# Optimization experiments

Hardware: AMD Instinct MI355X
Metric: run time of the kernel (lower is better)

Reference implementation:

```python
import jax, jax.numpy as jnp
import numpy as np

N_TOKENS = 16384
HIDDEN = 1024
FFN = 256
N_EXPERTS = 12
TOP_K = 3


def setup_inputs() -> dict:
    key = jax.random.key(0)
    ks = jax.random.split(key, 5)
    return {
        "hidden_states": jax.random.normal(ks[0], (N_TOKENS, HIDDEN), dtype=jnp.float32),
        "gate_w": jax.random.normal(ks[1], (N_EXPERTS, HIDDEN), dtype=jnp.float32) * 0.02,
        "w1": jax.random.normal(ks[2], (N_EXPERTS, FFN, HIDDEN), dtype=jnp.float32) * 0.02,
        "w2": jax.random.normal(ks[3], (N_EXPERTS, HIDDEN, FFN), dtype=jnp.float32) * 0.02,
        "w3": jax.random.normal(ks[4], (N_EXPERTS, FFN, HIDDEN), dtype=jnp.float32) * 0.02,
    }


def reference(hidden_states, gate_w, w1, w2, w3):
    # Eval mode: no jitter noise (module only applies it when self.training).
    n = hidden_states.shape[0]
    router_logits = hidden_states @ gate_w.T                       # [N, E]
    routing_weights = jax.nn.softmax(router_logits.astype(jnp.float32), axis=1)
    top_w, selected_experts = jax.lax.top_k(routing_weights, TOP_K)  # [N, K]
    top_w = top_w / jnp.sum(top_w, axis=-1, keepdims=True)
    top_w = top_w.astype(hidden_states.dtype)

    # Dense combine-weight matrix [N, E]: zero for unselected experts.
    combine = jnp.zeros((n, N_EXPERTS), dtype=hidden_states.dtype)
    combine = combine.at[jnp.arange(n)[:, None], selected_experts].add(top_w)

    # SwiGLU experts computed for all (token, expert) pairs; unselected pairs
    # are zeroed by the combine weights -> same math as gather/scatter loop.
    h1 = jnp.einsum('nd,efd->nef', hidden_states, w1)              # [N, E, F]
    h3 = jnp.einsum('nd,efd->nef', hidden_states, w3)              # [N, E, F]
    h = jax.nn.silu(h1) * h3
    h = h * combine[:, :, None]                                    # weight before combine
    final = jnp.einsum('nef,edf->nd', h, w2)                       # [N, D]

    flat_e = selected_experts.reshape(-1)
    flat_w = top_w.reshape(-1).astype(jnp.float32)
    importance = jnp.zeros((N_EXPERTS,), jnp.float32).at[flat_e].add(flat_w)
    # torch.std is unbiased (ddof=1)
    router_loss = jnp.std(importance, ddof=1)
    return final, router_logits, selected_experts, router_loss
```

## Files before the change

kernel.cpp:

```cpp
#include <hip/hip_runtime.h>
#include <hip/hip_bf16.h>

#define NT 16384
#define HID 1024
#define FFN_ 256
#define NE 12
#define TOPK 3

typedef float  float4x  __attribute__((ext_vector_type(4)));
typedef short  short8x  __attribute__((ext_vector_type(8)));

__device__ __forceinline__ unsigned short f2bf(float f) {
    unsigned u = __float_as_uint(f);
    u += 0x7fffu + ((u >> 16) & 1u);
    return (unsigned short)(u >> 16);
}
__device__ __forceinline__ float bf2f(unsigned short u) {
    return __uint_as_float(((unsigned)u) << 16);
}

__device__ __forceinline__ void gl2lds16(const void* g, void* l) {
    __builtin_amdgcn_global_load_lds(
        (const __attribute__((address_space(1))) unsigned int*)g,
        (__attribute__((address_space(3))) unsigned int*)l, 16, 0, 0);
}

__global__ __launch_bounds__(256) void router_cvt_kernel(
    const float* __restrict__ X, const float* __restrict__ G,
    const float* __restrict__ w1, const float* __restrict__ w3, const float* __restrict__ w2,
    unsigned short* __restrict__ o1, unsigned short* __restrict__ o3, unsigned short* __restrict__ o2,
    float* __restrict__ out_logits, float* __restrict__ out_sel,
    unsigned short* __restrict__ xb,
    int* __restrict__ sel_e, float* __restrict__ sel_w)
{
    __shared__ __align__(16) float gls[NE * HID];

    if (blockIdx.x < 768) {
        const float* s; unsigned short* d;
        int m = blockIdx.x >> 8;
        if (m == 0)      { s = w1; d = o1; }
        else if (m == 1) { s = w3; d = o3; }
        else             { s = w2; d = o2; }
        const int n4 = NE * FFN_ * HID / 4;
        for (int i = (blockIdx.x & 255) * 256 + threadIdx.x; i < n4; i += 65536) {
            float4 v = ((const float4*)s)[i];
            ushort4 o;
            o.x = f2bf(v.x); o.y = f2bf(v.y); o.z = f2bf(v.z); o.w = f2bf(v.w);
            ((ushort4*)d)[i] = o;
        }
        return;
    }

    const int bx = blockIdx.x - 768;
    for (int i = threadIdx.x; i < NE * HID / 4; i += 256)
        ((float4*)gls)[i] = ((const float4*)G)[i];
    __syncthreads();

    const int wave = threadIdx.x >> 6, lane = threadIdx.x & 63;
    const int t = bx * 4 + wave;

    float xr[16];
    const float* xt = X + (size_t)t * HID;
    unsigned short* xbt = xb + (size_t)t * HID;
#pragma unroll
    for (int j = 0; j < 4; j++) {
        float4 v = ((const float4*)xt)[j * 64 + lane];
        xr[j*4+0] = v.x; xr[j*4+1] = v.y; xr[j*4+2] = v.z; xr[j*4+3] = v.w;
        ushort4 o;
        o.x = f2bf(v.x); o.y = f2bf(v.y); o.z = f2bf(v.z); o.w = f2bf(v.w);
        ((ushort4*)xbt)[j * 64 + lane] = o;
    }

    float logit[NE];
#pragma unroll
    for (int e = 0; e < NE; e++) {
        float s = 0.f;
#pragma unroll
        for (int j = 0; j < 4; j++) {
            float4 g = ((const float4*)gls)[e * 256 + j * 64 + lane];
            s += xr[j*4+0]*g.x + xr[j*4+1]*g.y + xr[j*4+2]*g.z + xr[j*4+3]*g.w;
        }
#pragma unroll
        for (int d = 32; d; d >>= 1) s += __shfl_xor(s, d, 64);
        logit[e] = s;
    }

    if (lane == 0) {
        float m = logit[0];
#pragma unroll
        for (int e = 1; e < NE; e++) m = fmaxf(m, logit[e]);
#pragma unroll
        for (int e = 0; e < NE; e++) out_logits[(size_t)t * NE + e] = logit[e];

        bool used[NE];
#pragma unroll
        for (int e = 0; e < NE; e++) used[e] = false;
        int   sel[TOPK];
        float w[TOPK];
        float wsum = 0.f;
#pragma unroll
        for (int k = 0; k < TOPK; k++) {
            int best = -1; float bv = -1e30f;
            for (int e = 0; e < NE; e++)
                if (!used[e] && logit[e] > bv) { bv = logit[e]; best = e; }
            used[best] = true;
            sel[k] = best;
            w[k] = __expf(bv - m);
            wsum += w[k];
        }
        float inv = 1.f / wsum;
#pragma unroll
        for (int k = 0; k < TOPK; k++) {
            float wk = w[k] * inv;
            out_sel[(size_t)t * TOPK + k] = (float)sel[k];
            sel_e[t * TOPK + k] = sel[k];
            sel_w[t * TOPK + k] = wk;
        }
    }
}

__global__ __launch_bounds__(256) void hist_kernel(
    const int* __restrict__ sel_e, const float* __restrict__ sel_w,
    int* __restrict__ counts, float* __restrict__ importance)
{
    __shared__ int   lcnt[NE];
    __shared__ float limp[NE];
    const int tid = threadIdx.x;
    if (tid < NE) { lcnt[tid] = 0; limp[tid] = 0.f; }
    __syncthreads();
    const int t = blockIdx.x * 256 + tid;
#pragma unroll
    for (int k = 0; k < TOPK; k++) {
        int e = sel_e[t * TOPK + k];
        atomicAdd(&lcnt[e], 1);
        atomicAdd(&limp[e], sel_w[t * TOPK + k]);
    }
    __syncthreads();
    if (tid < NE) {
        atomicAdd(&counts[tid], lcnt[tid]);
        atomicAdd(&importance[tid], limp[tid]);
    }
}

__global__ void scan_loss(const int* __restrict__ counts, int* __restrict__ cursor,
                          int* __restrict__ offsets, int* __restrict__ tile_base,
                          const float* __restrict__ importance,
                          float* __restrict__ loss_out)
{
    if (threadIdx.x == 0) {
        int acc = 0, tb = 0;
        for (int e = 0; e < NE; e++) {
            offsets[e] = acc; cursor[e] = acc; tile_base[e] = tb;
            tb += (counts[e] + 127) >> 7;
            acc += counts[e];
        }
        offsets[NE] = acc;
        tile_base[NE] = tb;
        float mean = 0.f;
        for (int e = 0; e < NE; e++) mean += importance[e];
        mean /= (float)NE;
        float var = 0.f;
        for (int e = 0; e < NE; e++) { float d = importance[e] - mean; var += d * d; }
        var /= (float)(NE - 1);
        *loss_out = sqrtf(var);
    }
}

__global__ __launch_bounds__(256) void place_kernel(
    const int* __restrict__ sel_e, const float* __restrict__ sel_w,
    int* __restrict__ cursor, int* __restrict__ tok_ids, float* __restrict__ slot_w,
    int* __restrict__ inv3)
{
    __shared__ int lcnt[NE];
    __shared__ int lbase[NE];
    const int tid = threadIdx.x;
    if (tid < NE) lcnt[tid] = 0;
    __syncthreads();
    const int t = blockIdx.x * 256 + tid;
    int e[TOPK], r[TOPK];
#pragma unroll
    for (int k = 0; k < TOPK; k++) {
        e[k] = sel_e[t * TOPK + k];
        r[k] = atomicAdd(&lcnt[e[k]], 1);
    }
    __syncthreads();
    if (tid < NE) lbase[tid] = atomicAdd(&cursor[tid], lcnt[tid]);
    __syncthreads();
#pragma unroll
    for (int k = 0; k < TOPK; k++) {
        int pos = lbase[e[k]] + r[k];
        tok_ids[pos] = t;
        slot_w[pos] = sel_w[t * TOPK + k];
        inv3[t * TOPK + k] = pos;
    }
}

__global__ __launch_bounds__(256) void ffn1_kernel(
    const unsigned short* __restrict__ xb, const unsigned short* __restrict__ wb1,
    const unsigned short* __restrict__ wb3, const int* __restrict__ offsets,
    const int* __restrict__ tile_base,
    const int* __restrict__ tok_ids, const float* __restrict__ slot_w,
    unsigned short* __restrict__ H)
{
    const int bx = blockIdx.x;
    if (bx >= tile_base[NE]) return;
    int e = 0;
    while (bx >= tile_base[e + 1]) e++;
    const int base = offsets[e];
    const int count = offsets[e + 1] - base;
    const int m0 = (bx - tile_base[e]) << 7;
    const int n0 = blockIdx.y * 128;

    __shared__ __align__(16) unsigned short As[2][4096];
    __shared__ __align__(16) unsigned short B1s[2][4096];
    __shared__ __align__(16) unsigned short B3s[2][4096];
    __shared__ int   tids[128];
    __shared__ float wts[128];

    const int tid = threadIdx.x;
    if (tid < 128) {
        int s = m0 + tid;
        tids[tid] = (s < count) ? tok_ids[base + s] : 0;
        wts[tid]  = (s < count) ? slot_w[base + s] : 0.f;
    }
    __syncthreads();

    const int wave = tid >> 6, lane = tid & 63;
    const int wave_m = wave & 1, wave_n = wave >> 1;

    const int srow = wave * 32 + (lane >> 2);
    const int schunk = (((lane & 3) ^ ((srow >> 1) & 3)) << 3);
    const int tokA0 = tids[srow];
    const int tokA1 = tids[srow + 16];

    const unsigned short* asrc0 = xb + (size_t)tokA0 * HID + schunk;
    const unsigned short* asrc1 = xb + (size_t)tokA1 * HID + schunk;
    const unsigned short* b1p0 = wb1 + (size_t)(e * FFN_ + n0 + srow) * HID + schunk;
    const unsigned short* b1p1 = b1p0 + 16 * HID;
    const unsigned short* b3p0 = wb3 + (size_t)(e * FFN_ + n0 + srow) * HID + schunk;
    const unsigned short* b3p1 = b3p0 + 16 * HID;

    const int woff = wave * 2048;

#define FFN1_STAGE(p) do {                                             \
        char* aD  = (char*)&As[p][0]  + woff;                          \
        char* b1D = (char*)&B1s[p][0] + woff;                          \
        char* b3D = (char*)&B3s[p][0] + woff;                          \
        gl2lds16(asrc0, aD);  gl2lds16(asrc1, aD + 1024);              \
        gl2lds16(b1p0, b1D);  gl2lds16(b1p1, b1D + 1024);              \
        gl2lds16(b3p0, b3D);  gl2lds16(b3p1, b3D + 1024);              \
        asrc0 += 32; asrc1 += 32; b1p0 += 32; b1p1 += 32;              \
        b3p0 += 32; b3p1 += 32; } while (0)

    const int r15 = lane & 15;
    const int rchunk = (((lane >> 4) ^ ((r15 >> 1) & 3)) << 3);

    float4x acc1[4][4], acc3[4][4];
#pragma unroll
    for (int mi = 0; mi < 4; mi++)
#pragma unroll
        for (int ni = 0; ni < 4; ni++) {
            acc1[mi][ni] = (float4x){0.f, 0.f, 0.f, 0.f};
            acc3[mi][ni] = (float4x){0.f, 0.f, 0.f, 0.f};
        }

    FFN1_STAGE(0);
    for (int kk = 0; kk < HID / 32; kk++) {
        __syncthreads();
        if (kk + 1 < HID / 32) FFN1_STAGE((kk + 1) & 1);
        const int p = kk & 1;

        short8x a[4], b1f[4], b3f[4];
#pragma unroll
        for (int mi = 0; mi < 4; mi++)
            a[mi] = *(const short8x*)(&As[p][0] + (wave_m * 64 + mi * 16 + r15) * 32 + rchunk);
#pragma unroll
        for (int ni = 0; ni < 4; ni++) {
            b1f[ni] = *(const short8x*)(&B1s[p][0] + (wave_n * 64 + ni * 16 + r15) * 32 + rchunk);
            b3f[ni] = *(const short8x*)(&B3s[p][0] + (wave_n * 64 + ni * 16 + r15) * 32 + rchunk);
        }
#pragma unroll
        for (int mi = 0; mi < 4; mi++)
#pragma unroll
            for (int ni = 0; ni < 4; ni++) {
                acc1[mi][ni] = __builtin_amdgcn_mfma_f32_16x16x32_bf16(a[mi], b1f[ni], acc1[mi][ni], 0, 0, 0);
                acc3[mi][ni] = __builtin_amdgcn_mfma_f32_16x16x32_bf16(a[mi], b3f[ni], acc3[mi][ni], 0, 0, 0);
            }
    }
#undef FFN1_STAGE

    const int laneh = lane >> 4;
#pragma unroll
    for (int mi = 0; mi < 4; mi++)
#pragma unroll
        for (int ni = 0; ni < 4; ni++)
#pragma unroll
            for (int r = 0; r < 4; r++) {
                int ml = wave_m * 64 + mi * 16 + laneh * 4 + r;
                int s = m0 + ml;
                if (s < count) {
                    float v1 = acc1[mi][ni][r];
                    float v3 = acc3[mi][ni][r];
                    float h = v1 * (1.f / (1.f + __expf(-v1))) * v3 * wts[ml];
                    int n = n0 + wave_n * 64 + ni * 16 + r15;
                    H[(size_t)(base + s) * FFN_ + n] = f2bf(h);
                }
            }
}

__global__ __launch_bounds__(256) void ffn2_store(
    const unsigned short* __restrict__ H, const unsigned short* __restrict__ wb2,
    const int* __restrict__ offsets, const int* __restrict__ tile_base,
    unsigned short* __restrict__ Obuf, int co, int nc)
{
    const int bx = blockIdx.x;
    if (bx >= tile_base[NE]) return;
    int e = 0;
    while (bx >= tile_base[e + 1]) e++;
    const int base = offsets[e];
    const int count = offsets[e + 1] - base;
    const int m0 = (bx - tile_base[e]) << 7;
    const int n0g = co + blockIdx.y * 128;

    __shared__ __align__(16) unsigned short As[2][4096];
    __shared__ __align__(16) unsigned short Bs[2][4096];

    const int tid = threadIdx.x;
    const int wave = tid >> 6, lane = tid & 63;
    const int wave_m = wave & 1, wave_n = wave >> 1;

    const int srow = wave * 32 + (lane >> 2);
    const int schunk = (((lane & 3) ^ ((srow >> 1) & 3)) << 3);

    const unsigned short* a0 = H + (size_t)(base + m0 + srow) * FFN_ + schunk;
    const unsigned short* a1 = a0 + 16 * FFN_;
    const unsigned short* b0 = wb2 + (size_t)(e * HID + n0g + srow) * FFN_ + schunk;
    const unsigned short* b1 = b0 + 16 * FFN_;

    const int woff = wave * 2048;

#define FFN2_STAGE(p) do {                                             \
        char* aD = (char*)&As[p][0] + woff;                            \
        char* bD = (char*)&Bs[p][0] + woff;                            \
        gl2lds16(a0, aD);  gl2lds16(a1, aD + 1024);                    \
        gl2lds16(b0, bD);  gl2lds16(b1, bD + 1024);                    \
        a0 += 32; a1 += 32; b0 += 32; b1 += 32; } while (0)

    const int r15 = lane & 15;
    const int rchunk = (((lane >> 4) ^ ((r15 >> 1) & 3)) << 3);

    float4x acc[4][4];
#pragma unroll
    for (int mi = 0; mi < 4; mi++)
#pragma unroll
        for (int ni = 0; ni < 4; ni++) acc[mi][ni] = (float4x){0.f, 0.f, 0.f, 0.f};

    FFN2_STAGE(0);
    for (int kk = 0; kk < FFN_ / 32; kk++) {
        __syncthreads();
        if (kk + 1 < FFN_ / 32) FFN2_STAGE((kk + 1) & 1);
        const int p = kk & 1;

        short8x af[4], bf[4];
#pragma unroll
        for (int mi = 0; mi < 4; mi++)
            af[mi] = *(const short8x*)(&As[p][0] + (wave_m * 64 + mi * 16 + r15) * 32 + rchunk);
#pragma unroll
        for (int ni = 0; ni < 4; ni++)
            bf[ni] = *(const short8x*)(&Bs[p][0] + (wave_n * 64 + ni * 16 + r15) * 32 + rchunk);
#pragma unroll
        for (int mi = 0; mi < 4; mi++)
#pragma unroll
            for (int ni = 0; ni < 4; ni++)
                acc[mi][ni] = __builtin_amdgcn_mfma_f32_16x16x32_bf16(af[mi], bf[ni], acc[mi][ni], 0, 0, 0);
    }
#undef FFN2_STAGE

    const int laneh = lane >> 4;
#pragma unroll
    for (int mi = 0; mi < 4; mi++)
#pragma unroll
        for (int ni = 0; ni < 4; ni++)
#pragma unroll
            for (int r = 0; r < 4; r++) {
                int ml = wave_m * 64 + mi * 16 + laneh * 4 + r;
                int s = m0 + ml;
                if (s < count) {
                    int col = (n0g - co) + wave_n * 64 + ni * 16 + r15;
                    Obuf[(size_t)(base + s) * nc + col] = f2bf(acc[mi][ni][r]);
                }
            }
}

__global__ __launch_bounds__(256) void combine_kernel(
    const unsigned short* __restrict__ Obuf, const int* __restrict__ inv3,
    float* __restrict__ final_out, int co, int pt_shift)
{
    const int idx = blockIdx.x * 256 + threadIdx.x;
    const int per_t = 1 << pt_shift;
    const int t = idx >> pt_shift;
    const int c4 = idx & (per_t - 1);
    const int s0 = inv3[t * TOPK + 0];
    const int s1 = inv3[t * TOPK + 1];
    const int s2 = inv3[t * TOPK + 2];
    const ushort4* O = (const ushort4*)Obuf;
    ushort4 u0 = O[(size_t)s0 * per_t + c4];
    ushort4 u1 = O[(size_t)s1 * per_t + c4];
    ushort4 u2 = O[(size_t)s2 * per_t + c4];
    float4 r;
    r.x = bf2f(u0.x) + bf2f(u1.x) + bf2f(u2.x);
    r.y = bf2f(u0.y) + bf2f(u1.y) + bf2f(u2.y);
    r.z = bf2f(u0.z) + bf2f(u1.z) + bf2f(u2.z);
    r.w = bf2f(u0.w) + bf2f(u1.w) + bf2f(u2.w);
    ((float4*)(final_out + (size_t)t * HID + co))[c4] = r;
}

__global__ __launch_bounds__(256) void ffn2_atomic(
    const unsigned short* __restrict__ H, const unsigned short* __restrict__ wb2,
    const int* __restrict__ offsets, const int* __restrict__ tile_base,
    const int* __restrict__ tok_ids, float* __restrict__ final_out)
{
    const int bx = blockIdx.x;
    if (bx >= tile_base[NE]) return;
    int e = 0;
    while (bx >= tile_base[e + 1]) e++;
    const int base = offsets[e];
    const int count = offsets[e + 1] - base;
    const int m0 = (bx - tile_base[e]) << 7;
    const int n0 = blockIdx.y * 128;

    __shared__ __align__(16) unsigned short As[2][4096];
    __shared__ __align__(16) unsigned short Bs[2][4096];
    __shared__ int tids[128];

    const int tid = threadIdx.x;
    if (tid < 128) {
        int s = m0 + tid;
        tids[tid] = (s < count) ? tok_ids[base + s] : 0;
    }
    __syncthreads();

    const int wave = tid >> 6, lane = tid & 63;
    const int wave_m = wave & 1, wave_n = wave >> 1;

    const int srow = wave * 32 + (lane >> 2);
    const int schunk = (((lane & 3) ^ ((srow >> 1) & 3)) << 3);
    const unsigned short* a0 = H + (size_t)(base + m0 + srow) * FFN_ + schunk;
    const unsigned short* a1 = a0 + 16 * FFN_;
    const unsigned short* b0 = wb2 + (size_t)(e * HID + n0 + srow) * FFN_ + schunk;
    const unsigned short* b1 = b0 + 16 * FFN_;

    const int woff = wave * 2048;
#define FFN2A_STAGE(p) do {                                            \
        char* aD = (char*)&As[p][0] + woff;                            \
        char* bD = (char*)&Bs[p][0] + woff;                            \
        gl2lds16(a0, aD);  gl2lds16(a1, aD + 1024);                    \
        gl2lds16(b0, bD);  gl2lds16(b1, bD + 1024);                    \
        a0 += 32; a1 += 32; b0 += 32; b1 += 32; } while (0)

    const int r15 = lane & 15;
    const int rchunk = (((lane >> 4) ^ ((r15 >> 1) & 3)) << 3);

    float4x acc[4][4];
#pragma unroll
    for (int mi = 0; mi < 4; mi++)
#pragma unroll
        for (int ni = 0; ni < 4; ni++) acc[mi][ni] = (float4x){0.f, 0.f, 0.f, 0.f};

    FFN2A_STAGE(0);
    for (int kk = 0; kk < FFN_ / 32; kk++) {
        __syncthreads();
        if (kk + 1 < FFN_ / 32) FFN2A_STAGE((kk + 1) & 1);
        const int p = kk & 1;
        short8x af[4], bf[4];
#pragma unroll
        for (int mi = 0; mi < 4; mi++)
            af[mi] = *(const short8x*)(&As[p][0] + (wave_m * 64 + mi * 16 + r15) * 32 + rchunk);
#pragma unroll
        for (int ni = 0; ni < 4; ni++)
            bf[ni] = *(const short8x*)(&Bs[p][0] + (wave_n * 64 + ni * 16 + r15) * 32 + rchunk);
#pragma unroll
        for (int mi = 0; mi < 4; mi++)
#pragma unroll
            for (int ni = 0; ni < 4; ni++)
                acc[mi][ni] = __builtin_amdgcn_mfma_f32_16x16x32_bf16(af[mi], bf[ni], acc[mi][ni], 0, 0, 0);
    }
#undef FFN2A_STAGE

    const int laneh = lane >> 4;
#pragma unroll
    for (int mi = 0; mi < 4; mi++)
#pragma unroll
        for (int ni = 0; ni < 4; ni++)
#pragma unroll
            for (int r = 0; r < 4; r++) {
                int ml = wave_m * 64 + mi * 16 + laneh * 4 + r;
                int s = m0 + ml;
                if (s < count) {
                    int n = n0 + wave_n * 64 + ni * 16 + r15;
                    atomicAdd(final_out + (size_t)tids[ml] * HID + n, acc[mi][ni][r]);
                }
            }
}

extern "C" void kernel_launch(void* const* d_in, const int* in_sizes, int n_in,
                              void* d_out, int out_size, void* d_ws, size_t ws_size,
                              hipStream_t stream) {
    const float* X  = (const float*)d_in[0];
    const float* G  = (const float*)d_in[1];
    const float* w1 = (const float*)d_in[2];
    const float* w2 = (const float*)d_in[3];
    const float* w3 = (const float*)d_in[4];

    float* out = (float*)d_out;
    float* out_final  = out;
    float* out_logits = out + (size_t)NT * HID;
    float* out_sel    = out_logits + (size_t)NT * NE;
    float* out_loss   = out_sel + (size_t)NT * TOPK;

    char* ws = (char*)d_ws;
    int*   counts     = (int*)(ws + 0);
    int*   cursor     = (int*)(ws + 64);
    int*   offsets    = (int*)(ws + 128);
    float* importance = (float*)(ws + 192);
    int*   tile_base  = (int*)(ws + 256);
    int*   sel_e   = (int*)(ws + 512);
    float* sel_w   = (float*)(ws + 197120);
    int*   tok_ids = (int*)(ws + 393728);
    float* slot_w  = (float*)(ws + 590336);
    unsigned short* wb1 = (unsigned short*)(ws + 786944);
    unsigned short* wb3 = (unsigned short*)(ws + 7078400);
    unsigned short* wb2 = (unsigned short*)(ws + 13369856);
    unsigned short* H   = (unsigned short*)(ws + 19661312);
    int*  inv3          = (int*)(ws + 44892672);
    const size_t obase  = 45089280;
    unsigned short* Obuf = (unsigned short*)(ws + obase);

    unsigned short* xb = (unsigned short*)d_out;

    int nc = 0;
    if      (ws_size >= obase + (size_t)NT * TOPK * 1024 * 2) nc = 1024;
    else if (ws_size >= obase + (size_t)NT * TOPK * 512  * 2) nc = 512;
    else if (ws_size >= obase + (size_t)NT * TOPK * 256  * 2) nc = 256;

    hipMemsetAsync(ws, 0, 320, stream);
    router_cvt_kernel<<<768 + NT / 4, 256, 0, stream>>>(
        X, G, w1, w3, w2, wb1, wb3, wb2, out_logits, out_sel, xb, sel_e, sel_w);
    hist_kernel<<<NT / 256, 256, 0, stream>>>(sel_e, sel_w, counts, importance);
    scan_loss<<<1, 64, 0, stream>>>(counts, cursor, offsets, tile_base, importance, out_loss);
    place_kernel<<<NT / 256, 256, 0, stream>>>(sel_e, sel_w, cursor, tok_ids, slot_w, inv3);
    ffn1_kernel<<<dim3(400, 2), 256, 0, stream>>>(xb, wb1, wb3, offsets, tile_base,
                                                  tok_ids, slot_w, H);

    if (nc) {
        const int np = 1024 / nc;
        const int pt_shift = (nc == 1024) ? 8 : (nc == 512 ? 7 : 6);
        for (int p = 0; p < np; p++) {
            ffn2_store<<<dim3(400, nc / 128), 256, 0, stream>>>(
                H, wb2, offsets, tile_base, Obuf, p * nc, nc);
            combine_kernel<<<(NT << pt_shift) / 256, 256, 0, stream>>>(
                Obuf, inv3, out_final, p * nc, pt_shift);
        }
    } else {
        hipMemsetAsync(d_out, 0, (size_t)NT * HID * sizeof(float), stream);
        ffn2_atomic<<<dim3(400, 8), 256, 0, stream>>>(H, wb2, offsets, tile_base,
                                                      tok_ids, out_final);
    }
}
```

Measured before the change: 374.3 us.

## Triple-buffer FFN GEMM LDS pipelines and batch router tokens per wave

Both expert GEMM kernels move from a double-buffered LDS ring to a three-stage ring. Each iteration waits with an explicit vmcnt count plus a raw barrier, so two global-to-LDS loads stay in flight while a tile is computed, where before a full __syncthreads ran each k-step. The router kernel now has each wave handle 8 tokens in a loop, cutting the router grid from 4096 blocks to 512 and amortising the gate-weight LDS fill. In exchange, LDS use per block rises by half, which may lower occupancy, and the hand-counted waitcnt values must match the number of loads issued per stage.

```diff
diff --git a/kernel.cpp b/kernel.cpp
--- a/kernel.cpp
+++ b/kernel.cpp
@@ -57,64 +57,67 @@
     __syncthreads();
 
     const int wave = threadIdx.x >> 6, lane = threadIdx.x & 63;
-    const int t = bx * 4 + wave;
-
-    float xr[16];
-    const float* xt = X + (size_t)t * HID;
-    unsigned short* xbt = xb + (size_t)t * HID;
-#pragma unroll
-    for (int j = 0; j < 4; j++) {
-        float4 v = ((const float4*)xt)[j * 64 + lane];
-        xr[j*4+0] = v.x; xr[j*4+1] = v.y; xr[j*4+2] = v.z; xr[j*4+3] = v.w;
-        ushort4 o;
-        o.x = f2bf(v.x); o.y = f2bf(v.y); o.z = f2bf(v.z); o.w = f2bf(v.w);
-        ((ushort4*)xbt)[j * 64 + lane] = o;
-    }
-
-    float logit[NE];
-#pragma unroll
-    for (int e = 0; e < NE; e++) {
-        float s = 0.f;
+
+    for (int it = 0; it < 8; it++) {
+        const int t = bx * 32 + wave * 8 + it;
+
+        float xr[16];
+        const float* xt = X + (size_t)t * HID;
+        unsigned short* xbt = xb + (size_t)t * HID;
 #pragma unroll
         for (int j = 0; j < 4; j++) {
-            float4 g = ((const float4*)gls)[e * 256 + j * 64 + lane];
-            s += xr[j*4+0]*g.x + xr[j*4+1]*g.y + xr[j*4+2]*g.z + xr[j*4+3]*g.w;
-        }
-#pragma unroll
-        for (int d = 32; d; d >>= 1) s += __shfl_xor(s, d, 64);
-        logit[e] = s;
-    }
-
-    if (lane == 0) {
-        float m = logit[0];
-#pragma unroll
-        for (int e = 1; e < NE; e++) m = fmaxf(m, logit[e]);
-#pragma unroll
-        for (int e = 0; e < NE; e++) out_logits[(size_t)t * NE + e] = logit[e];
-
-        bool used[NE];
-#pragma unroll
-        for (int e = 0; e < NE; e++) used[e] = false;
-        int   sel[TOPK];
-        float w[TOPK];
-        float wsum = 0.f;
-#pragma unroll
-        for (int k = 0; k < TOPK; k++) {
-            int best = -1; float bv = -1e30f;
-            for (int e = 0; e < NE; e++)
-                if (!used[e] && logit[e] > bv) { bv = logit[e]; best = e; }
-            used[best] = true;
-            sel[k] = best;
-            w[k] = __expf(bv - m);
-            wsum += w[k];
-        }
-        float inv = 1.f / wsum;
-#pragma unroll
-        for (int k = 0; k < TOPK; k++) {
-            float wk = w[k] * inv;
-            out_sel[(size_t)t * TOPK + k] = (float)sel[k];
-            sel_e[t * TOPK + k] = sel[k];
-            sel_w[t * TOPK + k] = wk;
+            float4 v = ((const float4*)xt)[j * 64 + lane];
+            xr[j*4+0] = v.x; xr[j*4+1] = v.y; xr[j*4+2] = v.z; xr[j*4+3] = v.w;
+            ushort4 o;
+            o.x = f2bf(v.x); o.y = f2bf(v.y); o.z = f2bf(v.z); o.w = f2bf(v.w);
+            ((ushort4*)xbt)[j * 64 + lane] = o;
+        }
+
+        float logit[NE];
+#pragma unroll
+        for (int e = 0; e < NE; e++) {
+            float s = 0.f;
+#pragma unroll
+            for (int j = 0; j < 4; j++) {
+                float4 g = ((const float4*)gls)[e * 256 + j * 64 + lane];
+                s += xr[j*4+0]*g.x + xr[j*4+1]*g.y + xr[j*4+2]*g.z + xr[j*4+3]*g.w;
+            }
+#pragma unroll
+            for (int d = 32; d; d >>= 1) s += __shfl_xor(s, d, 64);
+            logit[e] = s;
+        }
+
+        if (lane == 0) {
+            float m = logit[0];
+#pragma unroll
+            for (int e = 1; e < NE; e++) m = fmaxf(m, logit[e]);
+#pragma unroll
+            for (int e = 0; e < NE; e++) out_logits[(size_t)t * NE + e] = logit[e];
+
+            bool used[NE];
+#pragma unroll
+            for (int e = 0; e < NE; e++) used[e] = false;
+            int   sel[TOPK];
+            float w[TOPK];
+            float wsum = 0.f;
+#pragma unroll
+            for (int k = 0; k < TOPK; k++) {
+                int best = -1; float bv = -1e30f;
+                for (int e = 0; e < NE; e++)
+                    if (!used[e] && logit[e] > bv) { bv = logit[e]; best = e; }
+                used[best] = true;
+                sel[k] = best;
+                w[k] = __expf(bv - m);
+                wsum += w[k];
+            }
+            float inv = 1.f / wsum;
+#pragma unroll
+            for (int k = 0; k < TOPK; k++) {
+                float wk = w[k] * inv;
+                out_sel[(size_t)t * TOPK + k] = (float)sel[k];
+                sel_e[t * TOPK + k] = sel[k];
+                sel_w[t * TOPK + k] = wk;
+            }
         }
     }
 }
@@ -211,9 +214,9 @@
     const int m0 = (bx - tile_base[e]) << 7;
     const int n0 = blockIdx.y * 128;
 
-    __shared__ __align__(16) unsigned short As[2][4096];
-    __shared__ __align__(16) unsigned short B1s[2][4096];
-    __shared__ __align__(16) unsigned short B3s[2][4096];
+    __shared__ __align__(16) unsigned short As[3][4096];
+    __shared__ __align__(16) unsigned short B1s[3][4096];
+    __shared__ __align__(16) unsigned short B3s[3][4096];
     __shared__ int   tids[128];
     __shared__ float wts[128];
 
@@ -230,16 +233,12 @@
 
     const int srow = wave * 32 + (lane >> 2);
     const int schunk = (((lane & 3) ^ ((srow >> 1) & 3)) << 3);
-    const int tokA0 = tids[srow];
-    const int tokA1 = tids[srow + 16];
-
-    const unsigned short* asrc0 = xb + (size_t)tokA0 * HID + schunk;
-    const unsigned short* asrc1 = xb + (size_t)tokA1 * HID + schunk;
+    const unsigned short* asrc0 = xb + (size_t)tids[srow] * HID + schunk;
+    const unsigned short* asrc1 = xb + (size_t)tids[srow + 16] * HID + schunk;
     const unsigned short* b1p0 = wb1 + (size_t)(e * FFN_ + n0 + srow) * HID + schunk;
     const unsigned short* b1p1 = b1p0 + 16 * HID;
     const unsigned short* b3p0 = wb3 + (size_t)(e * FFN_ + n0 + srow) * HID + schunk;
     const unsigned short* b3p1 = b3p0 + 16 * HID;
-
     const int woff = wave * 2048;
 
 #define FFN1_STAGE(p) do {                                             \
@@ -264,30 +263,38 @@
             acc3[mi][ni] = (float4x){0.f, 0.f, 0.f, 0.f};
         }
 
+#define FFN1_COMPUTE(p) do {                                                                  \
+        short8x a[4], b1f[4], b3f[4];                                                         \
+        _Pragma("unroll")                                                                     \
+        for (int mi = 0; mi < 4; mi++)                                                        \
+            a[mi] = *(const short8x*)(&As[p][0] + (wave_m * 64 + mi * 16 + r15) * 32 + rchunk); \
+        _Pragma("unroll")                                                                     \
+        for (int ni = 0; ni < 4; ni++) {                                                      \
+            b1f[ni] = *(const short8x*)(&B1s[p][0] + (wave_n * 64 + ni * 16 + r15) * 32 + rchunk); \
+            b3f[ni] = *(const short8x*)(&B3s[p][0] + (wave_n * 64 + ni * 16 + r15) * 32 + rchunk); \
+        }                                                                                     \
+        _Pragma("unroll")                                                                     \
+        for (int mi = 0; mi < 4; mi++)                                                        \
+            _Pragma("unroll")                                                                 \
+            for (int ni = 0; ni < 4; ni++) {                                                  \
+                acc1[mi][ni] = __builtin_amdgcn_mfma_f32_16x16x32_bf16(a[mi], b1f[ni], acc1[mi][ni], 0, 0, 0); \
+                acc3[mi][ni] = __builtin_amdgcn_mfma_f32_16x16x32_bf16(a[mi], b3f[ni], acc3[mi][ni], 0, 0, 0); \
+            } } while (0)
+
     FFN1_STAGE(0);
-    for (int kk = 0; kk < HID / 32; kk++) {
-        __syncthreads();
-        if (kk + 1 < HID / 32) FFN1_STAGE((kk + 1) & 1);
-        const int p = kk & 1;
-
-        short8x a[4], b1f[4], b3f[4];
-#pragma unroll
-        for (int mi = 0; mi < 4; mi++)
-            a[mi] = *(const short8x*)(&As[p][0] + (wave_m * 64 + mi * 16 + r15) * 32 + rchunk);
-#pragma unroll
-        for (int ni = 0; ni < 4; ni++) {
-            b1f[ni] = *(const short8x*)(&B1s[p][0] + (wave_n * 64 + ni * 16 + r15) * 32 + rchunk);
-            b3f[ni] = *(const short8x*)(&B3s[p][0] + (wave_n * 64 + ni * 16 + r15) * 32 + rchunk);
-        }
-#pragma unroll
-        for (int mi = 0; mi < 4; mi++)
-#pragma unroll
-            for (int ni = 0; ni < 4; ni++) {
-                acc1[mi][ni] = __builtin_amdgcn_mfma_f32_16x16x32_bf16(a[mi], b1f[ni], acc1[mi][ni], 0, 0, 0);
-                acc3[mi][ni] = __builtin_amdgcn_mfma_f32_16x16x32_bf16(a[mi], b3f[ni], acc3[mi][ni], 0, 0, 0);
-            }
-    }
+    FFN1_STAGE(1);
+    int pr = 0, ps = 2;
+    for (int j = 0; j < 31; j++) {
+        asm volatile("s_waitcnt vmcnt(6)" ::: "memory");
+        __builtin_amdgcn_s_barrier();
+        if (j < 30) { FFN1_STAGE(ps); ps = (ps == 2) ? 0 : ps + 1; }
+        FFN1_COMPUTE(pr); pr = (pr == 2) ? 0 : pr + 1;
+    }
+    asm volatile("s_waitcnt vmcnt(0)" ::: "memory");
+    __builtin_amdgcn_s_barrier();
+    FFN1_COMPUTE(pr);
 #undef FFN1_STAGE
+#undef FFN1_COMPUTE
 
     const int laneh = lane >> 4;
 #pragma unroll
@@ -322,8 +329,8 @@
     const int m0 = (bx - tile_base[e]) << 7;
     const int n0g = co + blockIdx.y * 128;
 
-    __shared__ __align__(16) unsigned short As[2][4096];
-    __shared__ __align__(16) unsigned short Bs[2][4096];
+    __shared__ __align__(16) unsigned short As[3][4096];
+    __shared__ __align__(16) unsigned short Bs[3][4096];
 
     const int tid = threadIdx.x;
     const int wave = tid >> 6, lane = tid & 63;
@@ -355,26 +362,36 @@
 #pragma unroll
         for (int ni = 0; ni < 4; ni++) acc[mi][ni] = (float4x){0.f, 0.f, 0.f, 0.f};
 
+#define FFN2_COMPUTE(p) do {                                                                  \
+        short8x af[4], bf[4];                                                                 \
+        _Pragma("unroll")                                                                     \
+        for (int mi = 0; mi < 4; mi++)                                                        \
+            af[mi] = *(const short8x*)(&As[p][0] + (wave_m * 64 + mi * 16 + r15) * 32 + rchunk); \
+        _Pragma("unroll")                                                                     \
+        for (int ni = 0; ni < 4; ni++)                                                        \
+            bf[ni] = *(const short8x*)(&Bs[p][0] + (wave_n * 64 + ni * 16 + r15) * 32 + rchunk); \
+        _Pragma("unroll")                                                                     \
+        for (int mi = 0; mi < 4; mi++)                                                        \
+            _Pragma("unroll")                                                                 \
+            for (int ni = 0; ni < 4; ni++)                                                    \
+                acc[mi][ni] = __builtin_amdgcn_mfma_f32_16x16x32_bf16(af[mi], bf[ni], acc[mi][ni], 0, 0, 0); \
+        } while (0)
+
+    __syncthreads();
     FFN2_STAGE(0);
-    for (int kk = 0; kk < FFN_ / 32; kk++) {
-        __syncthreads();
-        if (kk + 1 < FFN_ / 32) FFN2_STAGE((kk + 1) & 1);
-        const int p = kk & 1;
-
-        short8x af[4], bf[4];
-#pragma unroll
-        for (int mi = 0; mi < 4; mi++)
-            af[mi] = *(const short8x*)(&As[p][0] + (wave_m * 64 + mi * 16 + r15) * 32 + rchunk);
-#pragma unroll
-        for (int ni = 0; ni < 4; ni++)
-            bf[ni] = *(const short8x*)(&Bs[p][0] + (wave_n * 64 + ni * 16 + r15) * 32 + rchunk);
-#pragma unroll
-        for (int mi = 0; mi < 4; mi++)
-#pragma unroll
-            for (int ni = 0; ni < 4; ni++)
-                acc[mi][ni] = __builtin_amdgcn_mfma_f32_16x16x32_bf16(af[mi], bf[ni], acc[mi][ni], 0, 0, 0);
-    }
+    FFN2_STAGE(1);
+    int pr = 0, ps = 2;
+    for (int j = 0; j < 7; j++) {
+        asm volatile("s_waitcnt vmcnt(4)" ::: "memory");
+        __builtin_amdgcn_s_barrier();
+        if (j < 6) { FFN2_STAGE(ps); ps = (ps == 2) ? 0 : ps + 1; }
+        FFN2_COMPUTE(pr); pr = (pr == 2) ? 0 : pr + 1;
+    }
+    asm volatile("s_waitcnt vmcnt(0)" ::: "memory");
+    __builtin_amdgcn_s_barrier();
+    FFN2_COMPUTE(pr);
 #undef FFN2_STAGE
+#undef FFN2_COMPUTE
 
     const int laneh = lane >> 4;
 #pragma unroll
@@ -544,7 +561,7 @@
     else if (ws_size >= obase + (size_t)NT * TOPK * 256  * 2) nc = 256;
 
     hipMemsetAsync(ws, 0, 320, stream);
-    router_cvt_kernel<<<768 + NT / 4, 256, 0, stream>>>(
+    router_cvt_kernel<<<768 + 512, 256, 0, stream>>>(
         X, G, w1, w3, w2, wb1, wb3, wb2, out_logits, out_sel, xb, sel_e, sel_w);
     hist_kernel<<<NT / 256, 256, 0, stream>>>(sel_e, sel_w, counts, importance);
     scan_loss<<<1, 64, 0, stream>>>(counts, cursor, offsets, tile_base, importance, out_loss);
```

Result: slower. 440.9 us (+17.8%).
